# Kernel tuning notes

Measured on AMD Instinct MI355X. Metric: run time of the kernel, lower is better.

## Reference

```python
import jax, jax.numpy as jnp
import numpy as np
import math

D_MODEL = 1024
N_HEADS = 16
B, T = 4, 2048

def setup_inputs() -> dict:
    key = jax.random.key(0)
    ks = jax.random.split(key, 8)
    s = 0.02
    return {
        "x": jax.random.normal(ks[0], (B, T, D_MODEL), dtype=jnp.float32),
        "Wq": jax.random.normal(ks[1], (D_MODEL, D_MODEL), dtype=jnp.float32) * s,
        "bq": jnp.zeros((D_MODEL,), jnp.float32),
        "Wk": jax.random.normal(ks[2], (D_MODEL, D_MODEL), dtype=jnp.float32) * s,
        "bk": jnp.zeros((D_MODEL,), jnp.float32),
        "Wv": jax.random.normal(ks[3], (D_MODEL, D_MODEL), dtype=jnp.float32) * s,
        "bv": jnp.zeros((D_MODEL,), jnp.float32),
        "gamma": jnp.ones((D_MODEL,), jnp.float32),
        "beta": jnp.zeros((D_MODEL,), jnp.float32),
        "n_heads": N_HEADS,
    }

def reference(x, Wq, bq, Wk, bk, Wv, bv, gamma, beta, n_heads):
    Bx, Tx, D = x.shape
    dh = D // n_heads
    def split_heads(y):  # [B,T,D] -> [B,H,T,dh]
        return y.reshape(Bx, Tx, n_heads, dh).transpose(0, 2, 1, 3)
    q = split_heads(x @ Wq.T + bq)
    k = split_heads(x @ Wk.T + bk)
    v = split_heads(x @ Wv.T + bv)
    scale = 1.0 / math.sqrt(dh)
    scores = jnp.einsum('bhqd,bhkd->bhqk', q, k) * scale  # [B,H,T,T]
    # faithful to torch: tril ones, zeros -> -inf (the +1 on allowed entries
    # is a per-row constant and leaves softmax unchanged)
    tril = jnp.tril(jnp.ones((Tx, Tx), jnp.float32))
    mask = jnp.where(tril == 0, -jnp.inf, 1.0)
    att = jax.nn.softmax(scores + mask, axis=-1)
    out = jnp.einsum('bhqk,bhkd->bhqd', att, v)
    out = out.transpose(0, 2, 1, 3).reshape(Bx, Tx, D)
    y = out + x  # dropout in eval mode is identity
    mu = jnp.mean(y, axis=-1, keepdims=True)
    var = jnp.var(y, axis=-1, keepdims=True)
    return (y - mu) / jnp.sqrt(var + 1e-5) * gamma + beta
```

## Files before the change

### kernel.cpp

```cpp
#include <hip/hip_runtime.h>
#include <math.h>

#define D_MODEL 1024
#define N_HEADS 16
#define DH 64
#define BATCH 4
#define SEQ 2048

typedef short  s16x8 __attribute__((ext_vector_type(8)));
typedef __bf16 b16x8 __attribute__((ext_vector_type(8)));
typedef float  f32x4 __attribute__((ext_vector_type(4)));

__device__ __forceinline__ f32x4 mfma16(s16x8 a, s16x8 b, f32x4 c) {
    return __builtin_amdgcn_mfma_f32_16x16x32_bf16(
        __builtin_bit_cast(b16x8, a), __builtin_bit_cast(b16x8, b), c, 0, 0, 0);
}

__device__ __forceinline__ unsigned short f2bf(float f) {
    unsigned u = __float_as_uint(f);
    u += 0x7FFFu + ((u >> 16) & 1u);
    return (unsigned short)(u >> 16);
}

__global__ __launch_bounds__(256) void convert_bf16(
    const float* __restrict__ x,  const float* __restrict__ wq,
    const float* __restrict__ wk, const float* __restrict__ wv,
    unsigned short* __restrict__ xb,  unsigned short* __restrict__ wqb,
    unsigned short* __restrict__ wkb, unsigned short* __restrict__ wvb)
{
    size_t i4 = (size_t)blockIdx.x * 256 + threadIdx.x;
    const float* src; unsigned short* dst; size_t o;
    if      (i4 < 2097152)          { src = x;  dst = xb;  o = i4; }
    else if (i4 < 2097152 + 262144) { src = wq; dst = wqb; o = i4 - 2097152; }
    else if (i4 < 2097152 + 524288) { src = wk; dst = wkb; o = i4 - 2097152 - 262144; }
    else                            { src = wv; dst = wvb; o = i4 - 2097152 - 524288; }
    float4 v = ((const float4*)src)[o];
    ushort4 r;
    r.x = f2bf(v.x); r.y = f2bf(v.y); r.z = f2bf(v.z); r.w = f2bf(v.w);
    *(ushort4*)&dst[o * 4] = r;
}

__global__ __launch_bounds__(256) void qkv_mfma(
    const unsigned short* __restrict__ xb,
    const unsigned short* __restrict__ wqb, const unsigned short* __restrict__ wkb,
    const unsigned short* __restrict__ wvb,
    const float* __restrict__ bq, const float* __restrict__ bk,
    const float* __restrict__ bv,
    unsigned short* __restrict__ qws, unsigned short* __restrict__ kws,
    unsigned short* __restrict__ vws)
{
    const int z = blockIdx.z;
    const unsigned short* __restrict__ W = (z == 0) ? wqb : (z == 1) ? wkb : wvb;
    const float* __restrict__ bias       = (z == 0) ? bq  : (z == 1) ? bk  : bv;

    __shared__ __align__(16) short Xs[64][72];
    __shared__ __align__(16) short Ws[64][72];

    const int tid = threadIdx.x;
    const int lane = tid & 63, w = tid >> 6;
    const int c = lane & 15, g = lane >> 4;
    const int rowBase = blockIdx.y * 64;
    const int colBase = blockIdx.x * 64;
    const int lr = tid >> 3, lc = (tid & 7) * 8;

    f32x4 acc[4];
    #pragma unroll
    for (int t = 0; t < 4; ++t) acc[t] = (f32x4)0.0f;

    for (int kt = 0; kt < D_MODEL; kt += 64) {
        __syncthreads();
        *(s16x8*)&Xs[lr][lc]      = *(const s16x8*)&xb[(size_t)(rowBase + lr) * D_MODEL + kt + lc];
        *(s16x8*)&Xs[lr + 32][lc] = *(const s16x8*)&xb[(size_t)(rowBase + lr + 32) * D_MODEL + kt + lc];
        *(s16x8*)&Ws[lr][lc]      = *(const s16x8*)&W[(size_t)(colBase + lr) * D_MODEL + kt + lc];
        *(s16x8*)&Ws[lr + 32][lc] = *(const s16x8*)&W[(size_t)(colBase + lr + 32) * D_MODEL + kt + lc];
        __syncthreads();

        s16x8 a0 = *(const s16x8*)&Xs[w * 16 + c][g * 8];
        s16x8 a1 = *(const s16x8*)&Xs[w * 16 + c][32 + g * 8];
        #pragma unroll
        for (int t = 0; t < 4; ++t) {
            s16x8 b0 = *(const s16x8*)&Ws[t * 16 + c][g * 8];
            s16x8 b1 = *(const s16x8*)&Ws[t * 16 + c][32 + g * 8];
            acc[t] = mfma16(a0, b0, acc[t]);
            acc[t] = mfma16(a1, b1, acc[t]);
        }
    }

    const float qscale = (z == 0) ? 0.125f : 1.0f;
    #pragma unroll
    for (int t = 0; t < 4; ++t) {
        const int n = colBase + t * 16 + c;
        const int h = n >> 6, d = n & 63;
        const float bn = bias[n];
        #pragma unroll
        for (int r = 0; r < 4; ++r) {
            const int m  = rowBase + w * 16 + g * 4 + r;
            const int b  = m >> 11, tt = m & (SEQ - 1);
            const unsigned short bfv = f2bf((acc[t][r] + bn) * qscale);
            if (z == 2)
                vws[((size_t)(b * N_HEADS + h) * DH + d) * SEQ + tt] = bfv;
            else if (z == 0)
                qws[((size_t)(b * N_HEADS + h) * SEQ + tt) * DH + d] = bfv;
            else
                kws[((size_t)(b * N_HEADS + h) * SEQ + tt) * DH + d] = bfv;
        }
    }
}

__global__ __launch_bounds__(256) void attn_mfma(
    const unsigned short* __restrict__ qws, const unsigned short* __restrict__ kws,
    const unsigned short* __restrict__ vws, float* __restrict__ out)
{
    __shared__ __align__(16) short Ks[64][72];
    __shared__ __align__(16) short Vs[64][72];
    __shared__ __align__(16) short Ps[4][16][72];

    const int tid = threadIdx.x, lane = tid & 63, w = tid >> 6;
    const int bh = blockIdx.y;
    const int qb = gridDim.x - 1 - blockIdx.x;
    const int qbase = qb * 64;
    const int b = bh >> 4, h = bh & (N_HEADS - 1);

    const unsigned short* qp = qws + (size_t)bh * SEQ * DH;
    const unsigned short* kp = kws + (size_t)bh * SEQ * DH;
    const unsigned short* vp = vws + (size_t)bh * DH * SEQ;

    const int c = lane & 15, g = lane >> 4;
    const int qlo = qbase + w * 16;
    const int lr = tid >> 3, lc = (tid & 7) * 8;

    const s16x8 qa0 = *(const s16x8*)&qp[(size_t)(qlo + c) * DH + g * 8];
    const s16x8 qa1 = *(const s16x8*)&qp[(size_t)(qlo + c) * DH + 32 + g * 8];

    f32x4 O[4];
    #pragma unroll
    for (int t = 0; t < 4; ++t) O[t] = (f32x4)0.0f;
    float mrow[4] = {-1e30f, -1e30f, -1e30f, -1e30f};
    float lrow[4] = {0.f, 0.f, 0.f, 0.f};

    const int nch = qb + 1;
    for (int ch = 0; ch < nch; ++ch) {
        const int kc = ch * 64;
        __syncthreads();
        *(s16x8*)&Ks[lr][lc]      = *(const s16x8*)&kp[(size_t)(kc + lr) * DH + lc];
        *(s16x8*)&Ks[lr + 32][lc] = *(const s16x8*)&kp[(size_t)(kc + lr + 32) * DH + lc];
        *(s16x8*)&Vs[lr][lc]      = *(const s16x8*)&vp[(size_t)lr * SEQ + kc + lc];
        *(s16x8*)&Vs[lr + 32][lc] = *(const s16x8*)&vp[(size_t)(lr + 32) * SEQ + kc + lc];
        __syncthreads();

        f32x4 S[4];
        #pragma unroll
        for (int t = 0; t < 4; ++t) {
            S[t] = (f32x4)0.0f;
            s16x8 b0 = *(const s16x8*)&Ks[t * 16 + c][g * 8];
            s16x8 b1 = *(const s16x8*)&Ks[t * 16 + c][32 + g * 8];
            S[t] = mfma16(qa0, b0, S[t]);
            S[t] = mfma16(qa1, b1, S[t]);
        }

        if (kc + 63 > qlo) {
            #pragma unroll
            for (int t = 0; t < 4; ++t) {
                const int key = kc + t * 16 + c;
                #pragma unroll
                for (int r = 0; r < 4; ++r)
                    if (key > qlo + g * 4 + r) S[t][r] = -1e30f;
            }
        }

        float p[4][4];
        #pragma unroll
        for (int r = 0; r < 4; ++r) {
            float mx = fmaxf(fmaxf(S[0][r], S[1][r]), fmaxf(S[2][r], S[3][r]));
            #pragma unroll
            for (int off = 1; off < 16; off <<= 1)
                mx = fmaxf(mx, __shfl_xor(mx, off, 64));
            const float mn = fmaxf(mrow[r], mx);
            const float al = __expf(mrow[r] - mn);
            mrow[r] = mn;
            float ls = 0.f;
            #pragma unroll
            for (int t = 0; t < 4; ++t) {
                p[t][r] = __expf(S[t][r] - mn);
                ls += p[t][r];
            }
            #pragma unroll
            for (int off = 1; off < 16; off <<= 1)
                ls += __shfl_xor(ls, off, 64);
            lrow[r] = lrow[r] * al + ls;
            #pragma unroll
            for (int t = 0; t < 4; ++t) O[t][r] *= al;
        }

        #pragma unroll
        for (int t = 0; t < 4; ++t)
            #pragma unroll
            for (int r = 0; r < 4; ++r)
                Ps[w][g * 4 + r][t * 16 + c] = (short)f2bf(p[t][r]);

        s16x8 pa0 = *(const s16x8*)&Ps[w][c][g * 8];
        s16x8 pa1 = *(const s16x8*)&Ps[w][c][32 + g * 8];

        #pragma unroll
        for (int t = 0; t < 4; ++t) {
            s16x8 v0 = *(const s16x8*)&Vs[t * 16 + c][g * 8];
            s16x8 v1 = *(const s16x8*)&Vs[t * 16 + c][32 + g * 8];
            O[t] = mfma16(pa0, v0, O[t]);
            O[t] = mfma16(pa1, v1, O[t]);
        }
    }

    #pragma unroll
    for (int r = 0; r < 4; ++r) {
        const float inv = 1.0f / lrow[r];
        const int row = qlo + g * 4 + r;
        #pragma unroll
        for (int t = 0; t < 4; ++t)
            out[((size_t)(b * SEQ + row)) * D_MODEL + h * DH + t * 16 + c] = O[t][r] * inv;
    }
}

__global__ __launch_bounds__(256) void resid_ln(
    float* __restrict__ out, const float* __restrict__ x,
    const float* __restrict__ gamma, const float* __restrict__ beta)
{
    const int row = blockIdx.x;
    const int tid = threadIdx.x;
    const int lane = tid & 63;
    const int wid = tid >> 6;

    float4 y  = *(float4*)(out + (size_t)row * D_MODEL + tid * 4);
    float4 xv = *(const float4*)(x + (size_t)row * D_MODEL + tid * 4);
    y.x += xv.x; y.y += xv.y; y.z += xv.z; y.w += xv.w;

    float sum = y.x + y.y + y.z + y.w;
    float sq  = y.x * y.x + y.y * y.y + y.z * y.z + y.w * y.w;
    #pragma unroll
    for (int off = 32; off > 0; off >>= 1) {
        sum += __shfl_xor(sum, off, 64);
        sq  += __shfl_xor(sq, off, 64);
    }

    __shared__ float s1[4], s2[4];
    if (lane == 0) { s1[wid] = sum; s2[wid] = sq; }
    __syncthreads();
    sum = s1[0] + s1[1] + s1[2] + s1[3];
    sq  = s2[0] + s2[1] + s2[2] + s2[3];

    const float mu  = sum * (1.0f / D_MODEL);
    const float var = sq * (1.0f / D_MODEL) - mu * mu;
    const float rs  = rsqrtf(var + 1e-5f);

    float4 gm = *(const float4*)(gamma + tid * 4);
    float4 be = *(const float4*)(beta + tid * 4);
    y.x = (y.x - mu) * rs * gm.x + be.x;
    y.y = (y.y - mu) * rs * gm.y + be.y;
    y.z = (y.z - mu) * rs * gm.z + be.z;
    y.w = (y.w - mu) * rs * gm.w + be.w;
    *(float4*)(out + (size_t)row * D_MODEL + tid * 4) = y;
}

extern "C" void kernel_launch(void* const* d_in, const int* in_sizes, int n_in,
                              void* d_out, int out_size, void* d_ws, size_t ws_size,
                              hipStream_t stream) {
    const float* x     = (const float*)d_in[0];
    const float* Wq    = (const float*)d_in[1];
    const float* bq    = (const float*)d_in[2];
    const float* Wk    = (const float*)d_in[3];
    const float* bk    = (const float*)d_in[4];
    const float* Wv    = (const float*)d_in[5];
    const float* bv    = (const float*)d_in[6];
    const float* gamma = (const float*)d_in[7];
    const float* beta  = (const float*)d_in[8];
    float* out = (float*)d_out;

    unsigned short* xb  = (unsigned short*)d_ws;
    unsigned short* wqb = xb  + (size_t)BATCH * SEQ * D_MODEL;
    unsigned short* wkb = wqb + (size_t)D_MODEL * D_MODEL;
    unsigned short* wvb = wkb + (size_t)D_MODEL * D_MODEL;
    unsigned short* qws = wvb + (size_t)D_MODEL * D_MODEL;
    unsigned short* kws = qws + (size_t)BATCH * SEQ * D_MODEL;
    unsigned short* vws = kws + (size_t)BATCH * SEQ * D_MODEL;

    convert_bf16<<<11264, 256, 0, stream>>>(x, Wq, Wk, Wv, xb, wqb, wkb, wvb);

    dim3 g1(D_MODEL / 64, (BATCH * SEQ) / 64, 3);
    qkv_mfma<<<g1, 256, 0, stream>>>(xb, wqb, wkb, wvb, bq, bk, bv, qws, kws, vws);

    dim3 g2(SEQ / 64, BATCH * N_HEADS);
    attn_mfma<<<g2, 256, 0, stream>>>(qws, kws, vws, out);

    resid_ln<<<BATCH * SEQ, 256, 0, stream>>>(out, x, gamma, beta);
}
```

Measured before the change: 454.5 us.

## Enlarge QKV GEMM tiles to 128x128 with direct LDS loads, prefetch K/V in attention

The QKV projection GEMM now uses 128x128 output tiles per block, with each wave computing a 64x64 sub-tile through a 4x4 MFMA accumulator grid. Operand tiles are loaded with global_load_lds straight into unpadded LDS. This raises arithmetic intensity and cuts global load traffic per FLOP. The attention kernel also register-prefetches the next K/V chunk while computing the current one, to hide load latency. Risks: removing the padding brings LDS bank conflicts on the fragment reads, the larger accumulator set raises register pressure, and the QKV grid has fewer blocks.

```diff
diff --git a/kernel.cpp b/kernel.cpp
--- a/kernel.cpp
+++ b/kernel.cpp
@@ -10,6 +10,7 @@
 typedef short  s16x8 __attribute__((ext_vector_type(8)));
 typedef __bf16 b16x8 __attribute__((ext_vector_type(8)));
 typedef float  f32x4 __attribute__((ext_vector_type(4)));
+typedef unsigned int u32;
 
 __device__ __forceinline__ f32x4 mfma16(s16x8 a, s16x8 b, f32x4 c) {
     return __builtin_amdgcn_mfma_f32_16x16x32_bf16(
@@ -20,6 +21,13 @@
     unsigned u = __float_as_uint(f);
     u += 0x7FFFu + ((u >> 16) & 1u);
     return (unsigned short)(u >> 16);
+}
+
+__device__ __forceinline__ void gload_lds16(const unsigned short* g, short* l) {
+    __builtin_amdgcn_global_load_lds(
+        (const __attribute__((address_space(1))) u32*)g,
+        (__attribute__((address_space(3))) u32*)l,
+        16, 0, 0);
 }
 
 __global__ __launch_bounds__(256) void convert_bf16(
@@ -53,56 +61,71 @@
     const unsigned short* __restrict__ W = (z == 0) ? wqb : (z == 1) ? wkb : wvb;
     const float* __restrict__ bias       = (z == 0) ? bq  : (z == 1) ? bk  : bv;
 
-    __shared__ __align__(16) short Xs[64][72];
-    __shared__ __align__(16) short Ws[64][72];
+    __shared__ __align__(16) short Xs[128][64];
+    __shared__ __align__(16) short Bs[128][64];
 
     const int tid = threadIdx.x;
     const int lane = tid & 63, w = tid >> 6;
+    const int wr = w >> 1, wc = w & 1;
     const int c = lane & 15, g = lane >> 4;
-    const int rowBase = blockIdx.y * 64;
-    const int colBase = blockIdx.x * 64;
-    const int lr = tid >> 3, lc = (tid & 7) * 8;
-
-    f32x4 acc[4];
-    #pragma unroll
-    for (int t = 0; t < 4; ++t) acc[t] = (f32x4)0.0f;
+    const int rowBase = blockIdx.y * 128;
+    const int colBase = blockIdx.x * 128;
+
+    const int srow = lane >> 3, scol = (lane & 7) * 8;
+
+    f32x4 acc[4][4];
+    #pragma unroll
+    for (int m = 0; m < 4; ++m)
+        #pragma unroll
+        for (int n = 0; n < 4; ++n) acc[m][n] = (f32x4)0.0f;
 
     for (int kt = 0; kt < D_MODEL; kt += 64) {
         __syncthreads();
-        *(s16x8*)&Xs[lr][lc]      = *(const s16x8*)&xb[(size_t)(rowBase + lr) * D_MODEL + kt + lc];
-        *(s16x8*)&Xs[lr + 32][lc] = *(const s16x8*)&xb[(size_t)(rowBase + lr + 32) * D_MODEL + kt + lc];
-        *(s16x8*)&Ws[lr][lc]      = *(const s16x8*)&W[(size_t)(colBase + lr) * D_MODEL + kt + lc];
-        *(s16x8*)&Ws[lr + 32][lc] = *(const s16x8*)&W[(size_t)(colBase + lr + 32) * D_MODEL + kt + lc];
+        #pragma unroll
+        for (int j = 0; j < 4; ++j) {
+            const int r = j * 32 + w * 8;
+            gload_lds16(&xb[(size_t)(rowBase + r + srow) * D_MODEL + kt + scol], &Xs[r][0]);
+            gload_lds16(&W [(size_t)(colBase + r + srow) * D_MODEL + kt + scol], &Bs[r][0]);
+        }
         __syncthreads();
 
-        s16x8 a0 = *(const s16x8*)&Xs[w * 16 + c][g * 8];
-        s16x8 a1 = *(const s16x8*)&Xs[w * 16 + c][32 + g * 8];
-        #pragma unroll
-        for (int t = 0; t < 4; ++t) {
-            s16x8 b0 = *(const s16x8*)&Ws[t * 16 + c][g * 8];
-            s16x8 b1 = *(const s16x8*)&Ws[t * 16 + c][32 + g * 8];
-            acc[t] = mfma16(a0, b0, acc[t]);
-            acc[t] = mfma16(a1, b1, acc[t]);
+        #pragma unroll
+        for (int half = 0; half < 2; ++half) {
+            s16x8 a[4], b[4];
+            #pragma unroll
+            for (int m = 0; m < 4; ++m)
+                a[m] = *(const s16x8*)&Xs[wr * 64 + m * 16 + c][half * 32 + g * 8];
+            #pragma unroll
+            for (int n = 0; n < 4; ++n)
+                b[n] = *(const s16x8*)&Bs[wc * 64 + n * 16 + c][half * 32 + g * 8];
+            #pragma unroll
+            for (int m = 0; m < 4; ++m)
+                #pragma unroll
+                for (int n = 0; n < 4; ++n)
+                    acc[m][n] = mfma16(a[m], b[n], acc[m][n]);
         }
     }
 
     const float qscale = (z == 0) ? 0.125f : 1.0f;
     #pragma unroll
-    for (int t = 0; t < 4; ++t) {
-        const int n = colBase + t * 16 + c;
-        const int h = n >> 6, d = n & 63;
-        const float bn = bias[n];
-        #pragma unroll
-        for (int r = 0; r < 4; ++r) {
-            const int m  = rowBase + w * 16 + g * 4 + r;
-            const int b  = m >> 11, tt = m & (SEQ - 1);
-            const unsigned short bfv = f2bf((acc[t][r] + bn) * qscale);
-            if (z == 2)
-                vws[((size_t)(b * N_HEADS + h) * DH + d) * SEQ + tt] = bfv;
-            else if (z == 0)
-                qws[((size_t)(b * N_HEADS + h) * SEQ + tt) * DH + d] = bfv;
-            else
-                kws[((size_t)(b * N_HEADS + h) * SEQ + tt) * DH + d] = bfv;
+    for (int n = 0; n < 4; ++n) {
+        const int col = colBase + wc * 64 + n * 16 + c;
+        const int h = col >> 6, d = col & 63;
+        const float bn = bias[col];
+        #pragma unroll
+        for (int m = 0; m < 4; ++m) {
+            #pragma unroll
+            for (int r = 0; r < 4; ++r) {
+                const int row = rowBase + wr * 64 + m * 16 + g * 4 + r;
+                const int b  = row >> 11, tt = row & (SEQ - 1);
+                const unsigned short bfv = f2bf((acc[m][n][r] + bn) * qscale);
+                if (z == 2)
+                    vws[((size_t)(b * N_HEADS + h) * DH + d) * SEQ + tt] = bfv;
+                else if (z == 0)
+                    qws[((size_t)(b * N_HEADS + h) * SEQ + tt) * DH + d] = bfv;
+                else
+                    kws[((size_t)(b * N_HEADS + h) * SEQ + tt) * DH + d] = bfv;
+            }
         }
     }
 }
@@ -139,14 +162,28 @@
     float lrow[4] = {0.f, 0.f, 0.f, 0.f};
 
     const int nch = qb + 1;
+
+    s16x8 kreg0 = *(const s16x8*)&kp[(size_t)lr * DH + lc];
+    s16x8 kreg1 = *(const s16x8*)&kp[(size_t)(lr + 32) * DH + lc];
+    s16x8 vreg0 = *(const s16x8*)&vp[(size_t)lr * SEQ + lc];
+    s16x8 vreg1 = *(const s16x8*)&vp[(size_t)(lr + 32) * SEQ + lc];
+
     for (int ch = 0; ch < nch; ++ch) {
         const int kc = ch * 64;
         __syncthreads();
-        *(s16x8*)&Ks[lr][lc]      = *(const s16x8*)&kp[(size_t)(kc + lr) * DH + lc];
-        *(s16x8*)&Ks[lr + 32][lc] = *(const s16x8*)&kp[(size_t)(kc + lr + 32) * DH + lc];
-        *(s16x8*)&Vs[lr][lc]      = *(const s16x8*)&vp[(size_t)lr * SEQ + kc + lc];
-        *(s16x8*)&Vs[lr + 32][lc] = *(const s16x8*)&vp[(size_t)(lr + 32) * SEQ + kc + lc];
+        *(s16x8*)&Ks[lr][lc]      = kreg0;
+        *(s16x8*)&Ks[lr + 32][lc] = kreg1;
+        *(s16x8*)&Vs[lr][lc]      = vreg0;
+        *(s16x8*)&Vs[lr + 32][lc] = vreg1;
         __syncthreads();
+
+        if (ch + 1 < nch) {
+            const int kn = kc + 64;
+            kreg0 = *(const s16x8*)&kp[(size_t)(kn + lr) * DH + lc];
+            kreg1 = *(const s16x8*)&kp[(size_t)(kn + lr + 32) * DH + lc];
+            vreg0 = *(const s16x8*)&vp[(size_t)lr * SEQ + kn + lc];
+            vreg1 = *(const s16x8*)&vp[(size_t)(lr + 32) * SEQ + kn + lc];
+        }
 
         f32x4 S[4];
         #pragma unroll
@@ -284,7 +321,7 @@
 
     convert_bf16<<<11264, 256, 0, stream>>>(x, Wq, Wk, Wv, xb, wqb, wkb, wvb);
 
-    dim3 g1(D_MODEL / 64, (BATCH * SEQ) / 64, 3);
+    dim3 g1(D_MODEL / 128, (BATCH * SEQ) / 128, 3);
     qkv_mfma<<<g1, 256, 0, stream>>>(xb, wqb, wkb, wvb, bq, bk, bv, qws, kws, vws);
 
     dim3 g2(SEQ / 64, BATCH * N_HEADS);
```

Result: faster. 419.9 us (-7.6%).
